# Kernel optimization log

Hardware: AMD Instinct MI355X
Metric: run time of the kernel (lower is better)

## Reference

```python
import jax, jax.numpy as jnp
import numpy as np

N = 591   # number of drugs (hardcoded in the original module)
FD = 1024 # args.fd
E = 120000


def setup_inputs() -> dict:
    key = jax.random.key(0)
    ks = jax.random.split(key, 32)
    s = 1.0 / np.sqrt(FD).astype(np.float32)
    inp = {}
    inp['dm1'] = jax.random.normal(ks[0], (N, FD), jnp.float32)
    for i, v in enumerate(['t', 's', 'g']):
        inp['edges_' + v] = jax.random.randint(ks[1 + i], (2, E), 0, N)
        inp['ew_' + v] = jax.random.uniform(ks[4 + i], (E,), jnp.float32)
    for i, nm in enumerate(['t1', 't2', 's1', 's2', 'g1', 'g2']):
        inp['W_' + nm] = jax.random.normal(ks[7 + i], (FD, FD), jnp.float32) * s
        inp['b_' + nm] = jnp.zeros((FD,), jnp.float32)
    inp['fc1_w'] = jax.random.normal(ks[20], (30, 6), jnp.float32) * 0.4
    inp['fc1_b'] = jnp.zeros((30,), jnp.float32)
    inp['fc2_w'] = jax.random.normal(ks[21], (6, 30), jnp.float32) * 0.2
    inp['fc2_b'] = jnp.zeros((6,), jnp.float32)
    inp['conv_w'] = jax.random.normal(ks[22], (6,), jnp.float32) * 0.4
    inp['conv_b'] = jnp.zeros((), jnp.float32)
    return inp


def gcn(x, W, b, src, dst, ew):
    """PyG GCNConv: x@W, add self-loops (weight 1), symmetric norm, scatter-add, +bias."""
    xw = x @ W                                   # [N, FD]
    loop = jnp.arange(N)
    src2 = jnp.concatenate([src, loop])
    dst2 = jnp.concatenate([dst, loop])
    ew2 = jnp.concatenate([ew, jnp.ones((N,), ew.dtype)])
    deg = jax.ops.segment_sum(ew2, dst2, num_segments=N)
    dinv = jnp.where(deg > 0, jax.lax.rsqrt(deg), 0.0)
    norm = dinv[src2] * ew2 * dinv[dst2]         # [E+N]
    agg = jax.ops.segment_sum(norm[:, None] * xw[src2], dst2, num_segments=N)
    return agg + b


def reference(dm1, edges_t, ew_t, edges_s, ew_s, edges_g, ew_g,
              W_t1, b_t1, W_t2, b_t2, W_s1, b_s1, W_s2, b_s2,
              W_g1, b_g1, W_g2, b_g2,
              fc1_w, fc1_b, fc2_w, fc2_b, conv_w, conv_b):
    def two_layers(e, w, W1, b1, W2, b2):
        h1 = jax.nn.relu(gcn(dm1, W1, b1, e[0], e[1], w))
        h2 = jax.nn.relu(gcn(h1, W2, b2, e[0], e[1], w))
        return h1, h2

    t1, t2 = two_layers(edges_t, ew_t, W_t1, b_t1, W_t2, b_t2)
    s1, s2 = two_layers(edges_s, ew_s, W_s1, b_s1, W_s2, b_s2)
    g1, g2 = two_layers(edges_g, ew_g, W_g1, b_g1, W_g2, b_g2)

    # cat(dim=1).t().view(1, 6, FD, N)  ->  [6, FD, N]
    comb = jnp.stack([t1.T, t2.T, s1.T, s2.T, g1.T, g2.T], axis=0)

    # SE-style channel attention over the 6 channels
    pool = comb.mean(axis=(1, 2))                         # [6]
    h = jax.nn.relu(pool @ fc1_w.T + fc1_b)               # [30]
    a = jax.nn.sigmoid(h @ fc2_w.T + fc2_b)               # [6]
    att = jax.nn.relu(a[:, None, None] * comb)            # [6, FD, N]

    # 1x1 conv (6 -> 1 channel), then view(FD, N).t()
    y = jnp.einsum('c,cfn->fn', conv_w, att) + conv_b     # [FD, N]
    return y.T                                            # [N, FD]
```

## Files before the change

kernel.cpp:

```cpp
#include <hip/hip_runtime.h>

#define NDRUG 591
#define FDIM 1024
#define NEDGE 120000
#define MPAD 640
#define ASTRIDE 349281
#define ABSTRIDE (MPAD*MPAD)
#define HSTRIDE (MPAD*FDIM)
#define REAL (NDRUG*FDIM)
#define WSTRIDE (FDIM*FDIM)

typedef __attribute__((ext_vector_type(8))) short bf16x8;
typedef __attribute__((ext_vector_type(4))) float f32x4;
typedef __attribute__((ext_vector_type(4))) unsigned short u16x4;

static __device__ __forceinline__ unsigned short f2bf(float f) {
    unsigned u = __builtin_bit_cast(unsigned, f);
    u += 0x7fffu + ((u >> 16) & 1u);
    return (unsigned short)(u >> 16);
}
static __device__ __forceinline__ float bf2f(unsigned short h) {
    return __builtin_bit_cast(float, ((unsigned)h) << 16);
}

typedef const __attribute__((address_space(1))) unsigned int* gp1_t;
typedef __attribute__((address_space(3))) unsigned int* lp3_t;
static __device__ __forceinline__ void gload16(const void* g, unsigned short* l) {
    __builtin_amdgcn_global_load_lds((gp1_t)g, (lp3_t)l, 16, 0, 0);
}

__global__ void init_kernel(float* AmatF, float* scal) {
    int i = blockIdx.x * blockDim.x + threadIdx.x;
    const int TOT = 3 * ASTRIDE;
    int b = i * 4;
    if (b + 3 < TOT) {
        *(float4*)(AmatF + b) = make_float4(0.f, 0.f, 0.f, 0.f);
    } else if (b < TOT) {
        for (int j = b; j < TOT; ++j) AmatF[j] = 0.f;
    }
    if (i < 16) scal[i] = 0.f;
}

__global__ void scatter_kernel(const int* e_t, const float* w_t,
                               const int* e_s, const float* w_s,
                               const int* e_g, const float* w_g, float* AmatF) {
    int i = blockIdx.x * blockDim.x + threadIdx.x;
    const int PER = NEDGE + NDRUG;
    if (i >= 3 * PER) return;
    int g = i / PER, r = i - g * PER;
    float* Ag = AmatF + (long)g * ASTRIDE;
    if (r < NEDGE) {
        const int*   E_ = (g == 0) ? e_t : (g == 1) ? e_s : e_g;
        const float* W_ = (g == 0) ? w_t : (g == 1) ? w_s : w_g;
        int src = E_[r], dst = E_[NEDGE + r];
        atomicAdd(Ag + (long)dst * NDRUG + src, W_[r]);
    } else {
        int n = r - NEDGE;
        atomicAdd(Ag + (long)n * NDRUG + n, 1.0f);
    }
}

__global__ void rowdeg_kernel(const float* AmatF, float* dinv) {
    int r = blockIdx.x, g = blockIdx.y;
    const float* row = AmatF + (long)g * ASTRIDE + (long)r * NDRUG;
    float s = 0.f;
    for (int c = threadIdx.x; c < NDRUG; c += 64) s += row[c];
#pragma unroll
    for (int off = 32; off > 0; off >>= 1) s += __shfl_down(s, off);
    if (threadIdx.x == 0)
        dinv[g * NDRUG + r] = (s > 0.f) ? rsqrtf(s) : 0.f;
}

__global__ void conv_A(const float* AmatF, const float* dinv, unsigned short* Amatb) {
    int r = blockIdx.x, g = blockIdx.y;
    int t = threadIdx.x;
    if (t >= 160) return;
    int c = t * 4;
    u16x4 o = {0, 0, 0, 0};
    if (r < NDRUG) {
        const float* src = AmatF + (long)g * ASTRIDE + (long)r * NDRUG;
        const float* dv = dinv + g * NDRUG;
        float dr = dv[r];
#pragma unroll
        for (int j = 0; j < 4; j++) {
            int cc = c + j;
            if (cc < NDRUG) o[j] = f2bf(src[cc] * dv[cc] * dr);
        }
    }
    *(u16x4*)(Amatb + (long)g * ABSTRIDE + (long)r * MPAD + c) = o;
}

__global__ void conv_dm1(const float* dm1, unsigned short* dm1b) {
    int r = blockIdx.x;
    int c = threadIdx.x * 4;
    u16x4 o = {0, 0, 0, 0};
    if (r < NDRUG) {
        float4 v = *(const float4*)(dm1 + (long)r * FDIM + c);
        o[0] = f2bf(v.x); o[1] = f2bf(v.y); o[2] = f2bf(v.z); o[3] = f2bf(v.w);
    }
    *(u16x4*)(dm1b + (long)r * FDIM + c) = o;
}

__global__ void conv_w6(const float* w0, const float* w1, const float* w2,
                        const float* w3, const float* w4, const float* w5,
                        unsigned short* WTb) {
    __shared__ float s[32][33];
    int z = blockIdx.z;
    const float* W = (z == 0) ? w0 : (z == 1) ? w1 : (z == 2) ? w2
                   : (z == 3) ? w3 : (z == 4) ? w4 : w5;
    unsigned short* WT = WTb + (long)z * WSTRIDE;
    int n0 = blockIdx.x * 32, k0 = blockIdx.y * 32;
    int tx = threadIdx.x & 31, ty = threadIdx.x >> 5;
#pragma unroll
    for (int p = 0; p < 4; p++)
        s[ty + 8 * p][tx] = W[(long)(k0 + ty + 8 * p) * FDIM + n0 + tx];
    __syncthreads();
#pragma unroll
    for (int p = 0; p < 4; p++)
        WT[(long)(n0 + ty + 8 * p) * FDIM + k0 + tx] = f2bf(s[tx][ty + 8 * p]);
}

template <int EPI>
__global__ __launch_bounds__(256) void mfma_gemm(
    const unsigned short* __restrict__ Abase, long strideA, int ldaK,
    const unsigned short* __restrict__ Bbase, long strideB, int ldbK,
    const float* __restrict__ bias0, const float* __restrict__ bias1,
    const float* __restrict__ bias2,
    unsigned short* __restrict__ Cbase, long strideC, int ldC, int K,
    float* __restrict__ poolacc, int layer)
{
    __shared__ unsigned short ldsA[2][4096];
    __shared__ unsigned short ldsB[2][4096];
    __shared__ float red[4];

    const int g = blockIdx.z;
    const unsigned short* A = Abase + (long)g * strideA;
    const unsigned short* B = Bbase + (long)g * strideB;
    unsigned short* C = Cbase + (long)g * strideC;
    const float* bias = (g == 0) ? bias0 : (g == 1) ? bias1 : bias2;

    const int m0 = blockIdx.y * 64;
    const int n0 = blockIdx.x * 64;
    const int tid = threadIdx.x;
    const int w = tid >> 6, lane = tid & 63;
    const int l15 = lane & 15, lq = lane >> 4;
    const int wm = w >> 1, wn = w & 1;

    const int sr  = lane >> 3;
    const int kcs = 8 * ((lane & 7) ^ sr);
    const int segA0 = 2 * w, segA1 = 2 * w + 1;
    const int rA0 = segA0 * 8 + sr, rA1 = segA1 * 8 + sr;

    int offA[2][2], offB[2][2];
    {
        int ra0 = 32 * wm + l15, ra1 = ra0 + 16;
        int rb0 = 32 * wn + l15, rb1 = rb0 + 16;
        offA[0][0] = ra0 * 64 + ((lq    ) ^ (ra0 & 7)) * 8;
        offA[0][1] = ra0 * 64 + ((lq + 4) ^ (ra0 & 7)) * 8;
        offA[1][0] = ra1 * 64 + ((lq    ) ^ (ra1 & 7)) * 8;
        offA[1][1] = ra1 * 64 + ((lq + 4) ^ (ra1 & 7)) * 8;
        offB[0][0] = rb0 * 64 + ((lq    ) ^ (rb0 & 7)) * 8;
        offB[0][1] = rb0 * 64 + ((lq + 4) ^ (rb0 & 7)) * 8;
        offB[1][0] = rb1 * 64 + ((lq    ) ^ (rb1 & 7)) * 8;
        offB[1][1] = rb1 * 64 + ((lq + 4) ^ (rb1 & 7)) * 8;
    }

    f32x4 acc00 = {0.f, 0.f, 0.f, 0.f}, acc01 = {0.f, 0.f, 0.f, 0.f};
    f32x4 acc10 = {0.f, 0.f, 0.f, 0.f}, acc11 = {0.f, 0.f, 0.f, 0.f};

    const int nt = K >> 6;

#define STAGE(bf, k0c) do {                                                        \
    gload16(A + (long)(m0 + rA0) * ldaK + (k0c) + kcs, &ldsA[bf][segA0 * 512]);    \
    gload16(A + (long)(m0 + rA1) * ldaK + (k0c) + kcs, &ldsA[bf][segA1 * 512]);    \
    gload16(B + (long)(n0 + rA0) * ldbK + (k0c) + kcs, &ldsB[bf][segA0 * 512]);    \
    gload16(B + (long)(n0 + rA1) * ldbK + (k0c) + kcs, &ldsB[bf][segA1 * 512]);    \
} while (0)

    STAGE(0, 0);

    for (int t = 0; t < nt; ++t) {
        const int cur = t & 1;
        if (t + 1 < nt) {
            STAGE(cur ^ 1, (t + 1) << 6);
            asm volatile("s_waitcnt vmcnt(4)");
        } else {
            asm volatile("s_waitcnt vmcnt(0)");
        }
        __builtin_amdgcn_s_barrier();
        __builtin_amdgcn_sched_barrier(0);
        const unsigned short* pa = ldsA[cur];
        const unsigned short* pb = ldsB[cur];
        {
            bf16x8 a0 = *(const bf16x8*)(pa + offA[0][0]);
            bf16x8 a1 = *(const bf16x8*)(pa + offA[1][0]);
            bf16x8 b0 = *(const bf16x8*)(pb + offB[0][0]);
            bf16x8 b1 = *(const bf16x8*)(pb + offB[1][0]);
            acc00 = __builtin_amdgcn_mfma_f32_16x16x32_bf16(a0, b0, acc00, 0, 0, 0);
            acc01 = __builtin_amdgcn_mfma_f32_16x16x32_bf16(a0, b1, acc01, 0, 0, 0);
            acc10 = __builtin_amdgcn_mfma_f32_16x16x32_bf16(a1, b0, acc10, 0, 0, 0);
            acc11 = __builtin_amdgcn_mfma_f32_16x16x32_bf16(a1, b1, acc11, 0, 0, 0);
        }
        {
            bf16x8 a0 = *(const bf16x8*)(pa + offA[0][1]);
            bf16x8 a1 = *(const bf16x8*)(pa + offA[1][1]);
            bf16x8 b0 = *(const bf16x8*)(pb + offB[0][1]);
            bf16x8 b1 = *(const bf16x8*)(pb + offB[1][1]);
            acc00 = __builtin_amdgcn_mfma_f32_16x16x32_bf16(a0, b0, acc00, 0, 0, 0);
            acc01 = __builtin_amdgcn_mfma_f32_16x16x32_bf16(a0, b1, acc01, 0, 0, 0);
            acc10 = __builtin_amdgcn_mfma_f32_16x16x32_bf16(a1, b0, acc10, 0, 0, 0);
            acc11 = __builtin_amdgcn_mfma_f32_16x16x32_bf16(a1, b1, acc11, 0, 0, 0);
        }
        asm volatile("s_waitcnt lgkmcnt(0)");
        __builtin_amdgcn_sched_barrier(0);
        __builtin_amdgcn_s_barrier();
    }
#undef STAGE

    if (EPI == 0) {
#define TSTORE(accv, mo, no) do {                                   \
        int nn = n0 + 32 * wn + (no) * 16 + l15;                    \
        int mm = m0 + 32 * wm + (mo) * 16 + lq * 4;                 \
        u16x4 pk;                                                   \
        pk[0] = f2bf(accv[0]); pk[1] = f2bf(accv[1]);               \
        pk[2] = f2bf(accv[2]); pk[3] = f2bf(accv[3]);               \
        *(u16x4*)&C[(long)nn * ldC + mm] = pk;                      \
} while (0)
        TSTORE(acc00, 0, 0); TSTORE(acc01, 0, 1);
        TSTORE(acc10, 1, 0); TSTORE(acc11, 1, 1);
#undef TSTORE
    } else {
        float spool = 0.f;
#define NSTORE(accv, mo, no) do {                                   \
        int nn = n0 + 32 * wn + (no) * 16 + l15;                    \
        int mm = m0 + 32 * wm + (mo) * 16 + lq * 4;                 \
        float bs = bias[nn];                                        \
        _Pragma("unroll")                                           \
        for (int i = 0; i < 4; i++) {                               \
            float v = fmaxf(accv[i] + bs, 0.f);                     \
            C[(long)(mm + i) * ldC + nn] = f2bf(v);                 \
            if (mm + i < NDRUG) spool += v;                         \
        }                                                           \
} while (0)
        NSTORE(acc00, 0, 0); NSTORE(acc01, 0, 1);
        NSTORE(acc10, 1, 0); NSTORE(acc11, 1, 1);
#undef NSTORE
#pragma unroll
        for (int off = 32; off > 0; off >>= 1) spool += __shfl_down(spool, off);
        if (lane == 0) red[w] = spool;
        __syncthreads();
        if (tid == 0)
            atomicAdd(poolacc + 2 * g + layer, red[0] + red[1] + red[2] + red[3]);
    }
}

__global__ void mlp_kernel(const float* acc, const float* fc1w, const float* fc1b,
                           const float* fc2w, const float* fc2b, const float* convw,
                           float* wout) {
    __shared__ float hsh[30], plsh[6];
    int t = threadIdx.x;
    const float inv = 1.0f / (float)REAL;
    if (t < 6) plsh[t] = acc[t] * inv;
    __syncthreads();
    if (t < 30) {
        float s = fc1b[t];
#pragma unroll
        for (int c = 0; c < 6; c++) s += plsh[c] * fc1w[t * 6 + c];
        hsh[t] = fmaxf(s, 0.f);
    }
    __syncthreads();
    float hv = (t < 30) ? hsh[t] : 0.f;
    for (int j = 0; j < 6; j++) {
        float p = (t < 30) ? hv * fc2w[j * 30 + t] : 0.f;
#pragma unroll
        for (int off = 32; off > 0; off >>= 1) p += __shfl_down(p, off);
        if (t == 0) {
            float s = fc2b[j] + p;
            wout[j] = convw[j] / (1.f + expf(-s));
        }
    }
}

__global__ void combine_kernel(const unsigned short* h1b, const unsigned short* h2b,
                               const float* wv, const float* convb, float* out) {
    int i = blockIdx.x * 256 + threadIdx.x;
    const int nv = REAL / 8;
    if (i >= nv) return;
    float cb = convb[0];
    float r[8];
#pragma unroll
    for (int j = 0; j < 8; j++) r[j] = cb;
#define ACCCH(c, ptr) do {                                          \
        float wc = wv[c];                                           \
        bf16x8 v = *(const bf16x8*)((ptr) + (long)i * 8);           \
        _Pragma("unroll")                                           \
        for (int j = 0; j < 8; j++) r[j] += wc * bf2f((unsigned short)v[j]); \
} while (0)
    ACCCH(0, h1b);
    ACCCH(1, h2b);
    ACCCH(2, h1b + HSTRIDE);
    ACCCH(3, h2b + HSTRIDE);
    ACCCH(4, h1b + 2 * HSTRIDE);
    ACCCH(5, h2b + 2 * HSTRIDE);
#undef ACCCH
    float4 o0 = make_float4(r[0], r[1], r[2], r[3]);
    float4 o1 = make_float4(r[4], r[5], r[6], r[7]);
    *(float4*)(out + (long)i * 8) = o0;
    *(float4*)(out + (long)i * 8 + 4) = o1;
}

extern "C" void kernel_launch(void* const* d_in, const int* in_sizes, int n_in,
                              void* d_out, int out_size, void* d_ws, size_t ws_size,
                              hipStream_t stream) {
    const float* dm1 = (const float*)d_in[0];
    const int*   e_t = (const int*)d_in[1];
    const float* w_t = (const float*)d_in[2];
    const int*   e_s = (const int*)d_in[3];
    const float* w_s = (const float*)d_in[4];
    const int*   e_g = (const int*)d_in[5];
    const float* w_g = (const float*)d_in[6];
    const float* W_t1 = (const float*)d_in[7];
    const float* b_t1 = (const float*)d_in[8];
    const float* W_t2 = (const float*)d_in[9];
    const float* b_t2 = (const float*)d_in[10];
    const float* W_s1 = (const float*)d_in[11];
    const float* b_s1 = (const float*)d_in[12];
    const float* W_s2 = (const float*)d_in[13];
    const float* b_s2 = (const float*)d_in[14];
    const float* W_g1 = (const float*)d_in[15];
    const float* b_g1 = (const float*)d_in[16];
    const float* W_g2 = (const float*)d_in[17];
    const float* b_g2 = (const float*)d_in[18];
    const float* fc1w = (const float*)d_in[19];
    const float* fc1b = (const float*)d_in[20];
    const float* fc2w = (const float*)d_in[21];
    const float* fc2b = (const float*)d_in[22];
    const float* convw = (const float*)d_in[23];
    const float* convb = (const float*)d_in[24];
    float* out = (float*)d_out;

    char* base = (char*)d_ws;
    unsigned short* WTb = (unsigned short*)base;
    float* AmatF = (float*)base;
    unsigned short* h2b = (unsigned short*)(base + (size_t)3 * WSTRIDE * 2);
    size_t o = (size_t)6 * WSTRIDE * 2;
    float* dinv = (float*)(base + o); o += 8192;
    float* scal = (float*)(base + o); o += 256;
    unsigned short* dm1b  = (unsigned short*)(base + o); o += (size_t)MPAD * FDIM * 2;
    unsigned short* Amatb = (unsigned short*)(base + o); o += (size_t)3 * ABSTRIDE * 2;
    unsigned short* xwT   = (unsigned short*)(base + o); o += (size_t)3 * HSTRIDE * 2;
    unsigned short* h1b   = (unsigned short*)(base + o); o += (size_t)3 * HSTRIDE * 2;
    if (ws_size < o) return;

    init_kernel<<<(3 * ASTRIDE / 4 + 256) / 256, 256, 0, stream>>>(AmatF, scal);
    scatter_kernel<<<(3 * (NEDGE + NDRUG) + 255) / 256, 256, 0, stream>>>(
        e_t, w_t, e_s, w_s, e_g, w_g, AmatF);
    rowdeg_kernel<<<dim3(NDRUG, 3), 64, 0, stream>>>(AmatF, dinv);
    conv_A<<<dim3(MPAD, 3), 256, 0, stream>>>(AmatF, dinv, Amatb);
    conv_w6<<<dim3(32, 32, 6), 256, 0, stream>>>(
        W_t1, W_s1, W_g1, W_t2, W_s2, W_g2, WTb);
    conv_dm1<<<MPAD, 256, 0, stream>>>(dm1, dm1b);

    dim3 gg(FDIM / 64, MPAD / 64, 3);
    mfma_gemm<0><<<gg, 256, 0, stream>>>(
        dm1b, 0L, FDIM, WTb, (long)WSTRIDE, FDIM,
        nullptr, nullptr, nullptr, xwT, (long)HSTRIDE, MPAD, FDIM, scal, 0);
    mfma_gemm<1><<<gg, 256, 0, stream>>>(
        Amatb, (long)ABSTRIDE, MPAD, xwT, (long)HSTRIDE, MPAD,
        b_t1, b_s1, b_g1, h1b, (long)HSTRIDE, FDIM, MPAD, scal, 0);
    mfma_gemm<0><<<gg, 256, 0, stream>>>(
        h1b, (long)HSTRIDE, FDIM, WTb + (size_t)3 * WSTRIDE, (long)WSTRIDE, FDIM,
        nullptr, nullptr, nullptr, xwT, (long)HSTRIDE, MPAD, FDIM, scal, 0);
    mfma_gemm<1><<<gg, 256, 0, stream>>>(
        Amatb, (long)ABSTRIDE, MPAD, xwT, (long)HSTRIDE, MPAD,
        b_t2, b_s2, b_g2, h2b, (long)HSTRIDE, FDIM, MPAD, scal, 1);

    mlp_kernel<<<1, 64, 0, stream>>>(scal, fc1w, fc1b, fc2w, fc2b, convw, scal + 8);
    combine_kernel<<<(REAL / 8 + 255) / 256, 256, 0, stream>>>(h1b, h2b, scal + 8, convb, out);
}
```

Baseline: 219.0 us.

## Replace LDS-staged GEMM with register-streamed per-wave 32x64 MFMA tiles

The batched GEMM stops staging A and B tiles through LDS with global_load_lds and barriers. Instead each wavefront independently computes a 32x64 output tile, loading bf16 fragments straight from global memory into registers with a two-stage register double buffer. Grid layout changes to 240 blocks of 4 independent waves, and the pool reduction now does one atomic per wave instead of going through a shared-memory block reduction. The workspace layout is also rearranged so that WTb and h2b no longer alias AmatF. This removes barriers and LDS traffic, but each wave now rereads its operands from global memory/L2 without sharing them across the block.

```diff
diff --git a/kernel.cpp b/kernel.cpp
--- a/kernel.cpp
+++ b/kernel.cpp
@@ -23,21 +23,12 @@
     return __builtin_bit_cast(float, ((unsigned)h) << 16);
 }
 
-typedef const __attribute__((address_space(1))) unsigned int* gp1_t;
-typedef __attribute__((address_space(3))) unsigned int* lp3_t;
-static __device__ __forceinline__ void gload16(const void* g, unsigned short* l) {
-    __builtin_amdgcn_global_load_lds((gp1_t)g, (lp3_t)l, 16, 0, 0);
-}
-
 __global__ void init_kernel(float* AmatF, float* scal) {
     int i = blockIdx.x * blockDim.x + threadIdx.x;
     const int TOT = 3 * ASTRIDE;
     int b = i * 4;
-    if (b + 3 < TOT) {
-        *(float4*)(AmatF + b) = make_float4(0.f, 0.f, 0.f, 0.f);
-    } else if (b < TOT) {
-        for (int j = b; j < TOT; ++j) AmatF[j] = 0.f;
-    }
+    if (b + 3 < TOT) *(float4*)(AmatF + b) = make_float4(0.f, 0.f, 0.f, 0.f);
+    else if (b < TOT) { for (int j = b; j < TOT; ++j) AmatF[j] = 0.f; }
     if (i < 16) scal[i] = 0.f;
 }
 
@@ -52,8 +43,7 @@
     if (r < NEDGE) {
         const int*   E_ = (g == 0) ? e_t : (g == 1) ? e_s : e_g;
         const float* W_ = (g == 0) ? w_t : (g == 1) ? w_s : w_g;
-        int src = E_[r], dst = E_[NEDGE + r];
-        atomicAdd(Ag + (long)dst * NDRUG + src, W_[r]);
+        atomicAdd(Ag + (long)E_[NEDGE + r] * NDRUG + E_[r], W_[r]);
     } else {
         int n = r - NEDGE;
         atomicAdd(Ag + (long)n * NDRUG + n, 1.0f);
@@ -67,8 +57,7 @@
     for (int c = threadIdx.x; c < NDRUG; c += 64) s += row[c];
 #pragma unroll
     for (int off = 32; off > 0; off >>= 1) s += __shfl_down(s, off);
-    if (threadIdx.x == 0)
-        dinv[g * NDRUG + r] = (s > 0.f) ? rsqrtf(s) : 0.f;
+    if (threadIdx.x == 0) dinv[g * NDRUG + r] = (s > 0.f) ? rsqrtf(s) : 0.f;
 }
 
 __global__ void conv_A(const float* AmatF, const float* dinv, unsigned short* Amatb) {
@@ -112,16 +101,16 @@
     int n0 = blockIdx.x * 32, k0 = blockIdx.y * 32;
     int tx = threadIdx.x & 31, ty = threadIdx.x >> 5;
 #pragma unroll
-    for (int p = 0; p < 4; p++)
-        s[ty + 8 * p][tx] = W[(long)(k0 + ty + 8 * p) * FDIM + n0 + tx];
+    for (int q = 0; q < 4; q++)
+        s[ty + 8 * q][tx] = W[(long)(k0 + ty + 8 * q) * FDIM + n0 + tx];
     __syncthreads();
 #pragma unroll
-    for (int p = 0; p < 4; p++)
-        WT[(long)(n0 + ty + 8 * p) * FDIM + k0 + tx] = f2bf(s[tx][ty + 8 * p]);
+    for (int q = 0; q < 4; q++)
+        WT[(long)(n0 + ty + 8 * q) * FDIM + k0 + tx] = f2bf(s[tx][ty + 8 * q]);
 }
 
 template <int EPI>
-__global__ __launch_bounds__(256) void mfma_gemm(
+__global__ __launch_bounds__(256) void gemm_rs(
     const unsigned short* __restrict__ Abase, long strideA, int ldaK,
     const unsigned short* __restrict__ Bbase, long strideB, int ldbK,
     const float* __restrict__ bias0, const float* __restrict__ bias1,
@@ -129,128 +118,90 @@
     unsigned short* __restrict__ Cbase, long strideC, int ldC, int K,
     float* __restrict__ poolacc, int layer)
 {
-    __shared__ unsigned short ldsA[2][4096];
-    __shared__ unsigned short ldsB[2][4096];
-    __shared__ float red[4];
-
-    const int g = blockIdx.z;
+    const int wt = blockIdx.x * 4 + (threadIdx.x >> 6);
+    const int g = wt / 320, rem = wt - g * 320;
+    const int m0 = (rem >> 4) * 32;
+    const int n0 = (rem & 15) * 64;
+    const int lane = threadIdx.x & 63, l15 = lane & 15, lq = lane >> 4;
+
     const unsigned short* A = Abase + (long)g * strideA;
     const unsigned short* B = Bbase + (long)g * strideB;
     unsigned short* C = Cbase + (long)g * strideC;
     const float* bias = (g == 0) ? bias0 : (g == 1) ? bias1 : bias2;
 
-    const int m0 = blockIdx.y * 64;
-    const int n0 = blockIdx.x * 64;
-    const int tid = threadIdx.x;
-    const int w = tid >> 6, lane = tid & 63;
-    const int l15 = lane & 15, lq = lane >> 4;
-    const int wm = w >> 1, wn = w & 1;
-
-    const int sr  = lane >> 3;
-    const int kcs = 8 * ((lane & 7) ^ sr);
-    const int segA0 = 2 * w, segA1 = 2 * w + 1;
-    const int rA0 = segA0 * 8 + sr, rA1 = segA1 * 8 + sr;
-
-    int offA[2][2], offB[2][2];
-    {
-        int ra0 = 32 * wm + l15, ra1 = ra0 + 16;
-        int rb0 = 32 * wn + l15, rb1 = rb0 + 16;
-        offA[0][0] = ra0 * 64 + ((lq    ) ^ (ra0 & 7)) * 8;
-        offA[0][1] = ra0 * 64 + ((lq + 4) ^ (ra0 & 7)) * 8;
-        offA[1][0] = ra1 * 64 + ((lq    ) ^ (ra1 & 7)) * 8;
-        offA[1][1] = ra1 * 64 + ((lq + 4) ^ (ra1 & 7)) * 8;
-        offB[0][0] = rb0 * 64 + ((lq    ) ^ (rb0 & 7)) * 8;
-        offB[0][1] = rb0 * 64 + ((lq + 4) ^ (rb0 & 7)) * 8;
-        offB[1][0] = rb1 * 64 + ((lq    ) ^ (rb1 & 7)) * 8;
-        offB[1][1] = rb1 * 64 + ((lq + 4) ^ (rb1 & 7)) * 8;
-    }
-
-    f32x4 acc00 = {0.f, 0.f, 0.f, 0.f}, acc01 = {0.f, 0.f, 0.f, 0.f};
-    f32x4 acc10 = {0.f, 0.f, 0.f, 0.f}, acc11 = {0.f, 0.f, 0.f, 0.f};
-
-    const int nt = K >> 6;
-
-#define STAGE(bf, k0c) do {                                                        \
-    gload16(A + (long)(m0 + rA0) * ldaK + (k0c) + kcs, &ldsA[bf][segA0 * 512]);    \
-    gload16(A + (long)(m0 + rA1) * ldaK + (k0c) + kcs, &ldsA[bf][segA1 * 512]);    \
-    gload16(B + (long)(n0 + rA0) * ldbK + (k0c) + kcs, &ldsB[bf][segA0 * 512]);    \
-    gload16(B + (long)(n0 + rA1) * ldbK + (k0c) + kcs, &ldsB[bf][segA1 * 512]);    \
-} while (0)
-
-    STAGE(0, 0);
-
-    for (int t = 0; t < nt; ++t) {
-        const int cur = t & 1;
-        if (t + 1 < nt) {
-            STAGE(cur ^ 1, (t + 1) << 6);
-            asm volatile("s_waitcnt vmcnt(4)");
-        } else {
-            asm volatile("s_waitcnt vmcnt(0)");
-        }
-        __builtin_amdgcn_s_barrier();
-        __builtin_amdgcn_sched_barrier(0);
-        const unsigned short* pa = ldsA[cur];
-        const unsigned short* pb = ldsB[cur];
-        {
-            bf16x8 a0 = *(const bf16x8*)(pa + offA[0][0]);
-            bf16x8 a1 = *(const bf16x8*)(pa + offA[1][0]);
-            bf16x8 b0 = *(const bf16x8*)(pb + offB[0][0]);
-            bf16x8 b1 = *(const bf16x8*)(pb + offB[1][0]);
-            acc00 = __builtin_amdgcn_mfma_f32_16x16x32_bf16(a0, b0, acc00, 0, 0, 0);
-            acc01 = __builtin_amdgcn_mfma_f32_16x16x32_bf16(a0, b1, acc01, 0, 0, 0);
-            acc10 = __builtin_amdgcn_mfma_f32_16x16x32_bf16(a1, b0, acc10, 0, 0, 0);
-            acc11 = __builtin_amdgcn_mfma_f32_16x16x32_bf16(a1, b1, acc11, 0, 0, 0);
-        }
-        {
-            bf16x8 a0 = *(const bf16x8*)(pa + offA[0][1]);
-            bf16x8 a1 = *(const bf16x8*)(pa + offA[1][1]);
-            bf16x8 b0 = *(const bf16x8*)(pb + offB[0][1]);
-            bf16x8 b1 = *(const bf16x8*)(pb + offB[1][1]);
-            acc00 = __builtin_amdgcn_mfma_f32_16x16x32_bf16(a0, b0, acc00, 0, 0, 0);
-            acc01 = __builtin_amdgcn_mfma_f32_16x16x32_bf16(a0, b1, acc01, 0, 0, 0);
-            acc10 = __builtin_amdgcn_mfma_f32_16x16x32_bf16(a1, b0, acc10, 0, 0, 0);
-            acc11 = __builtin_amdgcn_mfma_f32_16x16x32_bf16(a1, b1, acc11, 0, 0, 0);
-        }
-        asm volatile("s_waitcnt lgkmcnt(0)");
-        __builtin_amdgcn_sched_barrier(0);
-        __builtin_amdgcn_s_barrier();
-    }
-#undef STAGE
+    const unsigned short* pa0 = A + (long)(m0 + l15) * ldaK + lq * 8;
+    const unsigned short* pa1 = pa0 + (long)16 * ldaK;
+    const unsigned short* pb0 = B + (long)(n0 + l15) * ldbK + lq * 8;
+    const unsigned short* pb1 = pb0 + (long)16 * ldbK;
+    const unsigned short* pb2 = pb0 + (long)32 * ldbK;
+    const unsigned short* pb3 = pb0 + (long)48 * ldbK;
+
+    f32x4 a00 = {0,0,0,0}, a01 = {0,0,0,0}, a02 = {0,0,0,0}, a03 = {0,0,0,0};
+    f32x4 a10 = {0,0,0,0}, a11 = {0,0,0,0}, a12 = {0,0,0,0}, a13 = {0,0,0,0};
+
+    bf16x8 a0c, a1c, b0c, b1c, b2c, b3c;
+    bf16x8 a0n, a1n, b0n, b1n, b2n, b3n;
+
+#define LOADF(sfx, kk) do {                         \
+    a0##sfx = *(const bf16x8*)(pa0 + (kk));         \
+    a1##sfx = *(const bf16x8*)(pa1 + (kk));         \
+    b0##sfx = *(const bf16x8*)(pb0 + (kk));         \
+    b1##sfx = *(const bf16x8*)(pb1 + (kk));         \
+    b2##sfx = *(const bf16x8*)(pb2 + (kk));         \
+    b3##sfx = *(const bf16x8*)(pb3 + (kk));         \
+} while (0)
+#define MFMA8(sfx) do {                                                         \
+    a00 = __builtin_amdgcn_mfma_f32_16x16x32_bf16(a0##sfx, b0##sfx, a00, 0,0,0);\
+    a01 = __builtin_amdgcn_mfma_f32_16x16x32_bf16(a0##sfx, b1##sfx, a01, 0,0,0);\
+    a02 = __builtin_amdgcn_mfma_f32_16x16x32_bf16(a0##sfx, b2##sfx, a02, 0,0,0);\
+    a03 = __builtin_amdgcn_mfma_f32_16x16x32_bf16(a0##sfx, b3##sfx, a03, 0,0,0);\
+    a10 = __builtin_amdgcn_mfma_f32_16x16x32_bf16(a1##sfx, b0##sfx, a10, 0,0,0);\
+    a11 = __builtin_amdgcn_mfma_f32_16x16x32_bf16(a1##sfx, b1##sfx, a11, 0,0,0);\
+    a12 = __builtin_amdgcn_mfma_f32_16x16x32_bf16(a1##sfx, b2##sfx, a12, 0,0,0);\
+    a13 = __builtin_amdgcn_mfma_f32_16x16x32_bf16(a1##sfx, b3##sfx, a13, 0,0,0);\
+} while (0)
+
+    LOADF(c, 0);
+    for (int kk = 0; kk < K; kk += 64) {
+        LOADF(n, kk + 32);
+        MFMA8(c);
+        if (kk + 64 < K) LOADF(c, kk + 64);
+        MFMA8(n);
+    }
+#undef LOADF
+#undef MFMA8
 
     if (EPI == 0) {
-#define TSTORE(accv, mo, no) do {                                   \
-        int nn = n0 + 32 * wn + (no) * 16 + l15;                    \
-        int mm = m0 + 32 * wm + (mo) * 16 + lq * 4;                 \
+#define TSTORE(accv, i, j) do {                                     \
+        int nn = n0 + (j) * 16 + l15;                               \
+        int mm = m0 + (i) * 16 + lq * 4;                            \
         u16x4 pk;                                                   \
         pk[0] = f2bf(accv[0]); pk[1] = f2bf(accv[1]);               \
         pk[2] = f2bf(accv[2]); pk[3] = f2bf(accv[3]);               \
         *(u16x4*)&C[(long)nn * ldC + mm] = pk;                      \
 } while (0)
-        TSTORE(acc00, 0, 0); TSTORE(acc01, 0, 1);
-        TSTORE(acc10, 1, 0); TSTORE(acc11, 1, 1);
+        TSTORE(a00, 0, 0); TSTORE(a01, 0, 1); TSTORE(a02, 0, 2); TSTORE(a03, 0, 3);
+        TSTORE(a10, 1, 0); TSTORE(a11, 1, 1); TSTORE(a12, 1, 2); TSTORE(a13, 1, 3);
 #undef TSTORE
     } else {
         float spool = 0.f;
-#define NSTORE(accv, mo, no) do {                                   \
-        int nn = n0 + 32 * wn + (no) * 16 + l15;                    \
-        int mm = m0 + 32 * wm + (mo) * 16 + lq * 4;                 \
+#define NSTORE(accv, i, j) do {                                     \
+        int nn = n0 + (j) * 16 + l15;                               \
+        int mm = m0 + (i) * 16 + lq * 4;                            \
         float bs = bias[nn];                                        \
         _Pragma("unroll")                                           \
-        for (int i = 0; i < 4; i++) {                               \
-            float v = fmaxf(accv[i] + bs, 0.f);                     \
-            C[(long)(mm + i) * ldC + nn] = f2bf(v);                 \
-            if (mm + i < NDRUG) spool += v;                         \
+        for (int r = 0; r < 4; r++) {                               \
+            float v = fmaxf(accv[r] + bs, 0.f);                     \
+            C[(long)(mm + r) * ldC + nn] = f2bf(v);                 \
+            if (mm + r < NDRUG) spool += v;                         \
         }                                                           \
 } while (0)
-        NSTORE(acc00, 0, 0); NSTORE(acc01, 0, 1);
-        NSTORE(acc10, 1, 0); NSTORE(acc11, 1, 1);
+        NSTORE(a00, 0, 0); NSTORE(a01, 0, 1); NSTORE(a02, 0, 2); NSTORE(a03, 0, 3);
+        NSTORE(a10, 1, 0); NSTORE(a11, 1, 1); NSTORE(a12, 1, 2); NSTORE(a13, 1, 3);
 #undef NSTORE
 #pragma unroll
         for (int off = 32; off > 0; off >>= 1) spool += __shfl_down(spool, off);
-        if (lane == 0) red[w] = spool;
-        __syncthreads();
-        if (tid == 0)
-            atomicAdd(poolacc + 2 * g + layer, red[0] + red[1] + red[2] + red[3]);
+        if (lane == 0) atomicAdd(poolacc + 2 * g + layer, spool);
     }
 }
 
@@ -271,13 +222,10 @@
     __syncthreads();
     float hv = (t < 30) ? hsh[t] : 0.f;
     for (int j = 0; j < 6; j++) {
-        float p = (t < 30) ? hv * fc2w[j * 30 + t] : 0.f;
-#pragma unroll
-        for (int off = 32; off > 0; off >>= 1) p += __shfl_down(p, off);
-        if (t == 0) {
-            float s = fc2b[j] + p;
-            wout[j] = convw[j] / (1.f + expf(-s));
-        }
+        float pr = (t < 30) ? hv * fc2w[j * 30 + t] : 0.f;
+#pragma unroll
+        for (int off = 32; off > 0; off >>= 1) pr += __shfl_down(pr, off);
+        if (t == 0) wout[j] = convw[j] / (1.f + expf(-(fc2b[j] + pr)));
     }
 }
 
@@ -287,14 +235,14 @@
     const int nv = REAL / 8;
     if (i >= nv) return;
     float cb = convb[0];
-    float r[8];
-#pragma unroll
-    for (int j = 0; j < 8; j++) r[j] = cb;
+    float r8[8];
+#pragma unroll
+    for (int j = 0; j < 8; j++) r8[j] = cb;
 #define ACCCH(c, ptr) do {                                          \
         float wc = wv[c];                                           \
         bf16x8 v = *(const bf16x8*)((ptr) + (long)i * 8);           \
         _Pragma("unroll")                                           \
-        for (int j = 0; j < 8; j++) r[j] += wc * bf2f((unsigned short)v[j]); \
+        for (int j = 0; j < 8; j++) r8[j] += wc * bf2f((unsigned short)v[j]); \
 } while (0)
     ACCCH(0, h1b);
     ACCCH(1, h2b);
@@ -303,75 +251,60 @@
     ACCCH(4, h1b + 2 * HSTRIDE);
     ACCCH(5, h2b + 2 * HSTRIDE);
 #undef ACCCH
-    float4 o0 = make_float4(r[0], r[1], r[2], r[3]);
-    float4 o1 = make_float4(r[4], r[5], r[6], r[7]);
-    *(float4*)(out + (long)i * 8) = o0;
-    *(float4*)(out + (long)i * 8 + 4) = o1;
+    *(float4*)(out + (long)i * 8)     = make_float4(r8[0], r8[1], r8[2], r8[3]);
+    *(float4*)(out + (long)i * 8 + 4) = make_float4(r8[4], r8[5], r8[6], r8[7]);
 }
 
 extern "C" void kernel_launch(void* const* d_in, const int* in_sizes, int n_in,
                               void* d_out, int out_size, void* d_ws, size_t ws_size,
                               hipStream_t stream) {
     const float* dm1 = (const float*)d_in[0];
-    const int*   e_t = (const int*)d_in[1];
-    const float* w_t = (const float*)d_in[2];
-    const int*   e_s = (const int*)d_in[3];
-    const float* w_s = (const float*)d_in[4];
-    const int*   e_g = (const int*)d_in[5];
-    const float* w_g = (const float*)d_in[6];
-    const float* W_t1 = (const float*)d_in[7];
-    const float* b_t1 = (const float*)d_in[8];
-    const float* W_t2 = (const float*)d_in[9];
-    const float* b_t2 = (const float*)d_in[10];
-    const float* W_s1 = (const float*)d_in[11];
-    const float* b_s1 = (const float*)d_in[12];
-    const float* W_s2 = (const float*)d_in[13];
-    const float* b_s2 = (const float*)d_in[14];
-    const float* W_g1 = (const float*)d_in[15];
-    const float* b_g1 = (const float*)d_in[16];
-    const float* W_g2 = (const float*)d_in[17];
-    const float* b_g2 = (const float*)d_in[18];
-    const float* fc1w = (const float*)d_in[19];
-    const float* fc1b = (const float*)d_in[20];
-    const float* fc2w = (const float*)d_in[21];
-    const float* fc2b = (const float*)d_in[22];
-    const float* convw = (const float*)d_in[23];
-    const float* convb = (const float*)d_in[24];
+    const int* et = (const int*)d_in[1];  const float* wt = (const float*)d_in[2];
+    const int* es = (const int*)d_in[3];  const float* ws = (const float*)d_in[4];
+    const int* eg = (const int*)d_in[5];  const float* wg = (const float*)d_in[6];
+    const float* W_t1 = (const float*)d_in[7];   const float* b_t1 = (const float*)d_in[8];
+    const float* W_t2 = (const float*)d_in[9];   const float* b_t2 = (const float*)d_in[10];
+    const float* W_s1 = (const float*)d_in[11];  const float* b_s1 = (const float*)d_in[12];
+    const float* W_s2 = (const float*)d_in[13];  const float* b_s2 = (const float*)d_in[14];
+    const float* W_g1 = (const float*)d_in[15];  const float* b_g1 = (const float*)d_in[16];
+    const float* W_g2 = (const float*)d_in[17];  const float* b_g2 = (const float*)d_in[18];
+    const float* fc1w = (const float*)d_in[19];  const float* fc1b = (const float*)d_in[20];
+    const float* fc2w = (const float*)d_in[21];  const float* fc2b = (const float*)d_in[22];
+    const float* convw = (const float*)d_in[23]; const float* convb = (const float*)d_in[24];
     float* out = (float*)d_out;
 
     char* base = (char*)d_ws;
-    unsigned short* WTb = (unsigned short*)base;
-    float* AmatF = (float*)base;
-    unsigned short* h2b = (unsigned short*)(base + (size_t)3 * WSTRIDE * 2);
-    size_t o = (size_t)6 * WSTRIDE * 2;
-    float* dinv = (float*)(base + o); o += 8192;
-    float* scal = (float*)(base + o); o += 256;
-    unsigned short* dm1b  = (unsigned short*)(base + o); o += (size_t)MPAD * FDIM * 2;
-    unsigned short* Amatb = (unsigned short*)(base + o); o += (size_t)3 * ABSTRIDE * 2;
-    unsigned short* xwT   = (unsigned short*)(base + o); o += (size_t)3 * HSTRIDE * 2;
-    unsigned short* h1b   = (unsigned short*)(base + o); o += (size_t)3 * HSTRIDE * 2;
+    size_t o = 0;
+    auto alloc = [&](size_t bytes) { void* p = base + o; o += (bytes + 255) & ~(size_t)255; return p; };
+    float* AmatF = (float*)alloc((size_t)3 * ASTRIDE * 4);
+    unsigned short* WTb   = (unsigned short*)alloc((size_t)6 * WSTRIDE * 2);
+    float* dinv  = (float*)alloc(8192);
+    float* scal  = (float*)alloc(256);
+    unsigned short* dm1b  = (unsigned short*)alloc((size_t)MPAD * FDIM * 2);
+    unsigned short* Amatb = (unsigned short*)alloc((size_t)3 * ABSTRIDE * 2);
+    unsigned short* xwT   = (unsigned short*)alloc((size_t)3 * HSTRIDE * 2);
+    unsigned short* h1b   = (unsigned short*)alloc((size_t)3 * HSTRIDE * 2);
+    unsigned short* h2b   = (unsigned short*)alloc((size_t)3 * HSTRIDE * 2);
     if (ws_size < o) return;
 
     init_kernel<<<(3 * ASTRIDE / 4 + 256) / 256, 256, 0, stream>>>(AmatF, scal);
     scatter_kernel<<<(3 * (NEDGE + NDRUG) + 255) / 256, 256, 0, stream>>>(
-        e_t, w_t, e_s, w_s, e_g, w_g, AmatF);
+        et, wt, es, ws, eg, wg, AmatF);
     rowdeg_kernel<<<dim3(NDRUG, 3), 64, 0, stream>>>(AmatF, dinv);
     conv_A<<<dim3(MPAD, 3), 256, 0, stream>>>(AmatF, dinv, Amatb);
-    conv_w6<<<dim3(32, 32, 6), 256, 0, stream>>>(
-        W_t1, W_s1, W_g1, W_t2, W_s2, W_g2, WTb);
+    conv_w6<<<dim3(32, 32, 6), 256, 0, stream>>>(W_t1, W_s1, W_g1, W_t2, W_s2, W_g2, WTb);
     conv_dm1<<<MPAD, 256, 0, stream>>>(dm1, dm1b);
 
-    dim3 gg(FDIM / 64, MPAD / 64, 3);
-    mfma_gemm<0><<<gg, 256, 0, stream>>>(
+    gemm_rs<0><<<240, 256, 0, stream>>>(
         dm1b, 0L, FDIM, WTb, (long)WSTRIDE, FDIM,
         nullptr, nullptr, nullptr, xwT, (long)HSTRIDE, MPAD, FDIM, scal, 0);
-    mfma_gemm<1><<<gg, 256, 0, stream>>>(
+    gemm_rs<1><<<240, 256, 0, stream>>>(
         Amatb, (long)ABSTRIDE, MPAD, xwT, (long)HSTRIDE, MPAD,
         b_t1, b_s1, b_g1, h1b, (long)HSTRIDE, FDIM, MPAD, scal, 0);
-    mfma_gemm<0><<<gg, 256, 0, stream>>>(
+    gemm_rs<0><<<240, 256, 0, stream>>>(
         h1b, (long)HSTRIDE, FDIM, WTb + (size_t)3 * WSTRIDE, (long)WSTRIDE, FDIM,
         nullptr, nullptr, nullptr, xwT, (long)HSTRIDE, MPAD, FDIM, scal, 0);
-    mfma_gemm<1><<<gg, 256, 0, stream>>>(
+    gemm_rs<1><<<240, 256, 0, stream>>>(
         Amatb, (long)ABSTRIDE, MPAD, xwT, (long)HSTRIDE, MPAD,
         b_t2, b_s2, b_g2, h2b, (long)HSTRIDE, FDIM, MPAD, scal, 1);
 
```

Measured after the change: 276.6 us. +26.3%, slower.
